# Optimization experiments

Measured on AMD Instinct MI355X. Metric: run time of the kernel, lower is better.

The kernel has to match this reference:

```python
import jax, jax.numpy as jnp
import numpy as np


def setup_inputs() -> dict:
    key = jax.random.key(0)
    k1, k2 = jax.random.split(key)
    B, S, D, N = 2, 2048, 1024, 16
    a = jax.random.uniform(k1, (B, S, D, N), dtype=jnp.float32)  # decay coeffs in [0,1)
    b = jax.random.normal(k2, (B, S, D, N), dtype=jnp.float32)
    return {"a": a, "b": b}


def reference(a, b):
    """h[t] = a[t] * h[t-1] + b[t], h[-1] = 0, computed via parallel associative scan.

    Associative op: (a1, b1) * (a2, b2) = (a1 * a2, a2 * b1 + b2).
    With h0 = 0, the running b-component equals h[t] exactly.
    """
    def combine(x, y):
        a1, b1 = x
        a2, b2 = y
        return a1 * a2, a2 * b1 + b2

    _, h = jax.lax.associative_scan(combine, (a, b), axis=1)
    return h  # (batch, seq_len, d_model, d_state)
```

## Files before the change

kernel.cpp:

```cpp
#include <hip/hip_runtime.h>


constexpr int S_LEN        = 2048;
constexpr int DN           = 1024 * 16;
constexpr long BATCH_STRIDE = (long)S_LEN * DN;
constexpr int NCHAIN       = 2 * DN;
constexpr int U            = 16;

__global__ __launch_bounds__(64) void scan_chain_kernel(
    const float* __restrict__ a,
    const float* __restrict__ b,
    float* __restrict__ out)
{
    const int m  = blockIdx.x * 64 + threadIdx.x;
    const int bi = m >> 14;
    const int dn = m & (DN - 1);
    const size_t base = (size_t)bi * BATCH_STRIDE + dn;

    const float* __restrict__ ap = a + base;
    const float* __restrict__ bp = b + base;
    float* __restrict__ op = out + base;

    float abuf[U], bbuf[U];
    #pragma unroll
    for (int u = 0; u < U; ++u) {
        abuf[u] = ap[(size_t)u * DN];
        bbuf[u] = bp[(size_t)u * DN];
    }

    float h = 0.0f;
    for (int s0 = 0; s0 < S_LEN; s0 += U) {
        float anxt[U], bnxt[U];
        const int nxt = s0 + U;
        if (nxt < S_LEN) {
            const float* __restrict__ ap2 = ap + (size_t)nxt * DN;
            const float* __restrict__ bp2 = bp + (size_t)nxt * DN;
            #pragma unroll
            for (int u = 0; u < U; ++u) {
                anxt[u] = ap2[(size_t)u * DN];
                bnxt[u] = bp2[(size_t)u * DN];
            }
        }

        float* __restrict__ op2 = op + (size_t)s0 * DN;
        #pragma unroll
        for (int u = 0; u < U; ++u) {
            h = fmaf(abuf[u], h, bbuf[u]);
            op2[(size_t)u * DN] = h;
        }

        #pragma unroll
        for (int u = 0; u < U; ++u) {
            abuf[u] = anxt[u];
            bbuf[u] = bnxt[u];
        }
    }
}

extern "C" void kernel_launch(void* const* d_in, const int* in_sizes, int n_in,
                              void* d_out, int out_size, void* d_ws, size_t ws_size,
                              hipStream_t stream) {
    const float* a = (const float*)d_in[0];
    const float* b = (const float*)d_in[1];
    float* out = (float*)d_out;

    dim3 grid(NCHAIN / 64);
    dim3 block(64);
    scan_chain_kernel<<<grid, block, 0, stream>>>(a, b, out);
}
```

Before: 586.5 us.

## Stage scan inputs through LDS with async global-to-LDS multi-buffered pipeline

Replaces the per-thread register double-buffering with 256-thread blocks that copy tiles of a and b straight into shared memory using global_load_lds 16-byte transfers. A 4-deep ring buffer keeps 3 tiles in flight, and manual vmcnt waits plus barriers synchronize each tile. The aim is to keep more memory traffic outstanding with fewer registers, raising bandwidth use on this memory-bound scan. In exchange it adds block-wide barriers per tile and depends on hand-tuned vmcnt counts, which also count the output stores.

```diff
diff --git a/kernel.cpp b/kernel.cpp
--- a/kernel.cpp
+++ b/kernel.cpp
@@ -1,58 +1,77 @@
 #include <hip/hip_runtime.h>
 
 
-constexpr int S_LEN        = 2048;
-constexpr int DN           = 1024 * 16;
-constexpr long BATCH_STRIDE = (long)S_LEN * DN;
-constexpr int NCHAIN       = 2 * DN;
-constexpr int U            = 16;
+constexpr int S_LEN = 2048;
+constexpr int DN = 1024 * 16;
+constexpr long long BATCH_STRIDE = (long long)S_LEN * DN;
+constexpr int CPB  = 256;
+constexpr int T    = 8;
+constexpr int NBUF = 4;
+constexpr int NT   = S_LEN / T;
+constexpr int NBLOCKS = (2 * DN) / CPB;
 
-__global__ __launch_bounds__(64) void scan_chain_kernel(
+template<int N>
+__device__ __forceinline__ void vmwait() {
+    asm volatile("s_waitcnt vmcnt(%0)" :: "n"(N) : "memory");
+}
+
+__device__ __forceinline__ void gload_lds16(const float* g, float* l) {
+    __builtin_amdgcn_global_load_lds(
+        (const __attribute__((address_space(1))) void*)g,
+        (__attribute__((address_space(3))) void*)l,
+        16 , 0, 0);
+}
+
+__global__ __launch_bounds__(256) void scan_lds_kernel(
     const float* __restrict__ a,
     const float* __restrict__ b,
     float* __restrict__ out)
 {
-    const int m  = blockIdx.x * 64 + threadIdx.x;
-    const int bi = m >> 14;
-    const int dn = m & (DN - 1);
-    const size_t base = (size_t)bi * BATCH_STRIDE + dn;
+    __shared__ float lds[NBUF * 2 * T * CPB];
 
-    const float* __restrict__ ap = a + base;
-    const float* __restrict__ bp = b + base;
-    float* __restrict__ op = out + base;
+    const int tid  = threadIdx.x;
+    const int lane = tid & 63;
+    const int wave = tid >> 6;
+    const int bi     = blockIdx.x >> 6;
+    const int chain0 = (blockIdx.x & 63) * CPB;
 
-    float abuf[U], bbuf[U];
-    #pragma unroll
-    for (int u = 0; u < U; ++u) {
-        abuf[u] = ap[(size_t)u * DN];
-        bbuf[u] = bp[(size_t)u * DN];
-    }
+    const size_t gband = (size_t)bi * BATCH_STRIDE + chain0;
+    const float* __restrict__ ga = a + gband;
+    const float* __restrict__ gb = b + gband;
+    float* __restrict__ go = out + gband + tid;
+
+    auto stage = [&](int tile) {
+        float* lb = &lds[(tile & (NBUF - 1)) * (2 * T * CPB)];
+        const size_t s0 = (size_t)tile * T;
+        #pragma unroll
+        for (int j = 0; j < 2; ++j) {
+            const int u = 2 * wave + j;
+            const size_t roff = (s0 + u) * (size_t)DN + (size_t)lane * 4;
+            gload_lds16(ga + roff, &lb[u * CPB]);
+            gload_lds16(gb + roff, &lb[(T + u) * CPB]);
+        }
+    };
+
+    stage(0); stage(1); stage(2);
 
     float h = 0.0f;
-    for (int s0 = 0; s0 < S_LEN; s0 += U) {
-        float anxt[U], bnxt[U];
-        const int nxt = s0 + U;
-        if (nxt < S_LEN) {
-            const float* __restrict__ ap2 = ap + (size_t)nxt * DN;
-            const float* __restrict__ bp2 = bp + (size_t)nxt * DN;
-            #pragma unroll
-            for (int u = 0; u < U; ++u) {
-                anxt[u] = ap2[(size_t)u * DN];
-                bnxt[u] = bp2[(size_t)u * DN];
-            }
-        }
+    for (int k = 0; k < NT; ++k) {
+        if      (k == 0)      vmwait<8>();
+        else if (k == 1)      vmwait<16>();
+        else if (k == 2)      vmwait<24>();
+        else if (k >= NT - 2) vmwait<24>();
+        else                  vmwait<32>();
+        __builtin_amdgcn_s_barrier();
+        __builtin_amdgcn_sched_barrier(0);
 
-        float* __restrict__ op2 = op + (size_t)s0 * DN;
+        if (k + 3 < NT) stage(k + 3);
+
+        const float* lb = &lds[(k & (NBUF - 1)) * (2 * T * CPB)];
+        float* orow = go + (size_t)k * T * DN;
         #pragma unroll
-        for (int u = 0; u < U; ++u) {
-            h = fmaf(abuf[u], h, bbuf[u]);
-            op2[(size_t)u * DN] = h;
-        }
-
-        #pragma unroll
-        for (int u = 0; u < U; ++u) {
-            abuf[u] = anxt[u];
-            bbuf[u] = bnxt[u];
+        for (int u = 0; u < T; ++u) {
+            h = fmaf(lb[u * CPB + tid], h, lb[(T + u) * CPB + tid]);
+            orow[(size_t)u * DN] = h;
         }
     }
 }
@@ -64,7 +83,7 @@
     const float* b = (const float*)d_in[1];
     float* out = (float*)d_out;
 
-    dim3 grid(NCHAIN / 64);
-    dim3 block(64);
-    scan_chain_kernel<<<grid, block, 0, stream>>>(a, b, out);
+    dim3 grid(NBLOCKS);
+    dim3 block(CPB);
+    scan_lds_kernel<<<grid, block, 0, stream>>>(a, b, out);
 }
```

Result: no change. 584.2 us (-0.4%).
